# Optimization experiments

Measured on AMD Instinct MI355X. Metric: run time of the kernel, lower is better.

The kernel has to match this reference:

```python
import jax, jax.numpy as jnp
import numpy as np

FM = 80            # feature_maps
N_ROUNDS = 32
NORM_EPS = 1e-3
LOSS_EPS = 1e-8


def _relu6(x):
    return jnp.clip(x, 0.0, 6.0)


def _norm(x):
    # tf.nn.moments over axis 0 + batch_normalization (no scale/offset)
    mean = jnp.mean(x, axis=0, keepdims=True)
    var = jnp.var(x, axis=0, keepdims=True)
    return (x - mean) * jax.lax.rsqrt(var + NORM_EPS)


def setup_inputs() -> dict:
    key = jax.random.key(0)
    n_vars, n_clauses, n_graphs, lits_per_clause = 100000, 420000, 100, 3
    n_cells = n_clauses * lits_per_clause
    ks = jax.random.split(key, 24)

    lit_var = jax.random.randint(ks[0], (n_cells,), 0, n_vars, dtype=jnp.int32)
    lit_neg = jax.random.randint(ks[1], (n_cells,), 0, 2, dtype=jnp.int32)
    clause_idx = jnp.repeat(jnp.arange(n_clauses, dtype=jnp.int32), lits_per_clause)
    clause_graph = jnp.repeat(jnp.arange(n_graphs, dtype=jnp.int32), n_clauses // n_graphs)

    def dense(k, fi, fo):
        return jax.random.normal(k, (fi, fo), jnp.float32) / np.sqrt(fi)

    inp = dict(
        lit_var=lit_var, lit_neg=lit_neg, clause_idx=clause_idx, clause_graph=clause_graph,
        n_vars=n_vars, n_clauses=n_clauses, n_graphs=n_graphs,
        L_init_scale=jnp.float32(1.0 / np.sqrt(FM)),
        C_init_scale=jnp.float32(1.0 / np.sqrt(FM)),
        LC_scale=jnp.float32(0.1), CL_scale=jnp.float32(0.1),
        # L_update MLP: in=3*FM (L, CL_msgs, flip(L)) -> hidden 3*FM relu6 -> FM
        Lu_W0=dense(ks[2], 3 * FM, 3 * FM), Lu_b0=jnp.zeros((3 * FM,), jnp.float32),
        Lu_W1=dense(ks[3], 3 * FM, FM),     Lu_b1=jnp.zeros((FM,), jnp.float32),
        # C_update MLP: in=2*FM (C, LC_msgs) -> hidden 2*FM relu6 -> FM
        Cu_W0=dense(ks[4], 2 * FM, 2 * FM), Cu_b0=jnp.zeros((2 * FM,), jnp.float32),
        Cu_W1=dense(ks[5], 2 * FM, FM),     Cu_b1=jnp.zeros((FM,), jnp.float32),
        # V_score MLP: in=2*FM -> 3 hidden relu6 layers of 2*FM -> 1
        Vs_W0=dense(ks[6], 2 * FM, 2 * FM), Vs_b0=jnp.zeros((2 * FM,), jnp.float32),
        Vs_W1=dense(ks[7], 2 * FM, 2 * FM), Vs_b1=jnp.zeros((2 * FM,), jnp.float32),
        Vs_W2=dense(ks[8], 2 * FM, 2 * FM), Vs_b2=jnp.zeros((2 * FM,), jnp.float32),
        Vs_W3=dense(ks[9], 2 * FM, 1),      Vs_b3=jnp.zeros((1,), jnp.float32),
    )
    return inp


def reference(lit_var, lit_neg, clause_idx, clause_graph, n_vars, n_clauses, n_graphs,
              L_init_scale, C_init_scale, LC_scale, CL_scale,
              Lu_W0, Lu_b0, Lu_W1, Lu_b1,
              Cu_W0, Cu_b0, Cu_W1, Cu_b1,
              Vs_W0, Vs_b0, Vs_W1, Vs_b1, Vs_W2, Vs_b2, Vs_W3, Vs_b3):
    n_lits = 2 * n_vars
    lit_row = lit_var + lit_neg * n_vars          # row in L for each cell
    sign = (1 - 2 * lit_neg).astype(jnp.float32)  # +1 positive literal, -1 negated

    def mlp_L(x):
        return _relu6(x @ Lu_W0 + Lu_b0) @ Lu_W1 + Lu_b1

    def mlp_C(x):
        return _relu6(x @ Cu_W0 + Cu_b0) @ Cu_W1 + Cu_b1

    def v_score(x):
        h = _relu6(x @ Vs_W0 + Vs_b0)
        h = _relu6(h @ Vs_W1 + Vs_b1)
        h = _relu6(h @ Vs_W2 + Vs_b2)
        return h @ Vs_W3 + Vs_b3

    def flip(L):
        return jnp.concatenate([L[n_vars:], L[:n_vars]], axis=0)

    def per_round_loss(logits):
        # softplus_mixed_loss over ragged clauses of signed literals
        lit_vals = logits[lit_var, 0] * sign                         # [n_cells]
        clause_sum = jax.ops.segment_sum(jax.nn.softplus(lit_vals), clause_idx,
                                         num_segments=n_clauses)     # [n_clauses]
        vc = jnp.exp(-clause_sum)
        per_clause = vc * (-jnp.log(1.0 - vc + LOSS_EPS))
        per_graph = jax.ops.segment_sum(per_clause, clause_graph, num_segments=n_graphs)
        return jnp.sum(jnp.sqrt(per_graph + 1e-6))

    L0 = jnp.ones((n_lits, FM), jnp.float32) * L_init_scale
    C0 = jnp.ones((n_clauses, FM), jnp.float32) * C_init_scale

    def round_fn(carry, _):
        L, C, loss = carry
        # CL^T @ L  (sparse gather + segment-sum over clause cells)
        LC_msgs = jax.ops.segment_sum(L[lit_row], clause_idx, num_segments=n_clauses) * LC_scale
        C = _norm(mlp_C(jnp.concatenate([C, LC_msgs], axis=-1)))
        # adj @ C  (scatter-add clause features back to literal rows)
        CL_msgs = jax.ops.segment_sum(C[clause_idx], lit_row, num_segments=n_lits) * CL_scale
        L = _norm(mlp_L(jnp.concatenate([L, CL_msgs, flip(L)], axis=-1)))
        V = jnp.concatenate([L[:n_vars], L[n_vars:]], axis=1)        # [n_vars, 2*FM]
        logits = v_score(V)
        loss = loss + per_round_loss(logits)
        return (L, C, loss), None

    (L, C, loss), _ = jax.lax.scan(round_fn, (L0, C0, jnp.float32(0.0)), None, length=N_ROUNDS)
    # final-round logits (recomputed from the final L state, identical math)
    logits = v_score(jnp.concatenate([L[:n_vars], L[n_vars:]], axis=1))
    return logits, loss / N_ROUNDS
```

## Files before the change

kernel.cpp:

```cpp
#include <hip/hip_runtime.h>
#include <hip/hip_fp8.h>
#include <math.h>


#define NROUNDS 32
#define NORM_EPS 1e-3f
#define LOSS_EPS 1e-8f

static constexpr int NV_CONST = 100000;
static constexpr int NG_CONST = 100;

typedef __attribute__((ext_vector_type(8))) short short8;
typedef __attribute__((ext_vector_type(8))) unsigned char uchar8;
typedef __attribute__((ext_vector_type(16))) unsigned char uchar16;
typedef __attribute__((ext_vector_type(4))) float f32x4;

__device__ __forceinline__ short f2bf(float f) {
    union { float f; unsigned u; } x; x.f = f;
    unsigned r = x.u + 0x7fffu + ((x.u >> 16) & 1u);
    return (short)(r >> 16);
}
__device__ __forceinline__ float bf2f(short s) {
    union { unsigned u; float f; } x; x.u = ((unsigned)(unsigned short)s) << 16;
    return x.f;
}
__device__ __forceinline__ unsigned char f2q8(float f) {
    f = fminf(fmaxf(f, -448.f), 448.f);
    __hip_fp8_e4m3 t(f);
    return t.__x;
}
__device__ __forceinline__ float q82f(unsigned char b) {
    __hip_fp8_e4m3 t; t.__x = b;
    return (float)t;
}


__global__ void k_zero_i(int* __restrict__ p, int n) {
    int i = blockIdx.x * 256 + threadIdx.x;
    if (i < n) p[i] = 0;
}
__global__ void k_fill_b(short* __restrict__ p, int n, const float* __restrict__ vp) {
    int i = blockIdx.x * 256 + threadIdx.x;
    if (i < n) p[i] = f2bf(*vp);
}
__global__ void k_fill_q8(unsigned char* __restrict__ p, int n, const float* __restrict__ vp) {
    int i = blockIdx.x * 256 + threadIdx.x;
    if (i < n) p[i] = f2q8(*vp);
}
__global__ void k_copy_int(int* __restrict__ dst, const int* __restrict__ src, int n) {
    int i = blockIdx.x * 256 + threadIdx.x;
    if (i < n) dst[i] = src[i];
}
__global__ void k_init_slabs(float* __restrict__ slabC, float* __restrict__ slabL,
                             float* __restrict__ loss_a, float nclf) {
    int i = blockIdx.x * 256 + threadIdx.x;
    if (i < 33 * 160) {
        slabC[i] = (i >= 80 && i < 160) ? nclf * (1.f - NORM_EPS) : 0.f;
        slabL[i] = 0.f;
    }
    if (i == 0) loss_a[0] = 0.f;
}

__global__ void k_litrow(const int* __restrict__ lit_var, const int* __restrict__ lit_neg,
                         int* __restrict__ litrow, int* __restrict__ lofs,
                         int* __restrict__ counts, int ncell, int nv) {
    int i = blockIdx.x * 256 + threadIdx.x;
    if (i < ncell) {
        int r = lit_var[i] + lit_neg[i] * nv;
        litrow[i] = r;
        lofs[i] = (r < nv) ? r * 20 : (r - nv) * 20 + 10;
        atomicAdd(&counts[r], 1);
    }
}

__launch_bounds__(1024)
__global__ void k_scan4(const int* __restrict__ counts, int* __restrict__ row_ptr,
                        int n, int total) {
    __shared__ int sd[1024];
    __shared__ int carry;
    int tid = threadIdx.x;
    if (tid == 0) carry = 0;
    __syncthreads();
    for (int base = 0; base < n; base += 4096) {
        int i0 = base + tid * 4;
        int a0 = (i0 + 0 < n) ? counts[i0 + 0] : 0;
        int a1 = (i0 + 1 < n) ? counts[i0 + 1] : 0;
        int a2 = (i0 + 2 < n) ? counts[i0 + 2] : 0;
        int a3 = (i0 + 3 < n) ? counts[i0 + 3] : 0;
        int s = a0 + a1 + a2 + a3;
        sd[tid] = s;
        __syncthreads();
        for (int off = 1; off < 1024; off <<= 1) {
            int t = (tid >= off) ? sd[tid - off] : 0;
            __syncthreads();
            sd[tid] += t;
            __syncthreads();
        }
        int excl = carry + sd[tid] - s;
        if (i0 + 0 < n) row_ptr[i0 + 0] = excl;
        if (i0 + 1 < n) row_ptr[i0 + 1] = excl + a0;
        if (i0 + 2 < n) row_ptr[i0 + 2] = excl + a0 + a1;
        if (i0 + 3 < n) row_ptr[i0 + 3] = excl + a0 + a1 + a2;
        __syncthreads();
        if (tid == 0) carry += sd[1023];
        __syncthreads();
    }
    if (tid == 0) row_ptr[n] = total;
}

__global__ void k_fill_csr(const int* __restrict__ litrow, const int* __restrict__ clause_idx,
                           int* __restrict__ cursor, int* __restrict__ cl_of, int ncell) {
    int i = blockIdx.x * 256 + threadIdx.x;
    if (i < ncell) {
        int r = litrow[i];
        int pos = atomicAdd(&cursor[r], 1);
        cl_of[pos] = clause_idx[i];
    }
}

__global__ void k_pack_w(const float* __restrict__ W, short* __restrict__ Wp,
                         int K, int N, int KB, int NB) {
    int t = blockIdx.x * 256 + threadIdx.x;
    int tot = NB * KB * 64;
    if (t >= tot) return;
    int lane = t & 63;
    int kb = (t >> 6) % KB;
    int nb = t / (64 * KB);
    int quad = lane >> 4, l15 = lane & 15;
    int n = nb * 16 + l15;
#pragma unroll
    for (int j = 0; j < 8; ++j) {
        int k = kb * 32 + quad * 8 + j;
        float f = (k < K && n < N) ? W[(size_t)k * N + n] : 0.f;
        Wp[(size_t)t * 8 + j] = f2bf(f);
    }
}


template <int KB, int NB>
__device__ __forceinline__ void mfma_layer(const short* lds, int SK,
                                           const short8* __restrict__ Wp,
                                           f32x4* acc, int lane, int arow) {
    const int quad8 = (lane >> 4) * 8;
    short8 a[KB];
#pragma unroll
    for (int kb = 0; kb < KB; ++kb)
        a[kb] = *(const short8*)(lds + arow * SK + kb * 32 + quad8);
#pragma unroll
    for (int kb = 0; kb < KB; ++kb)
#pragma unroll
        for (int nb = 0; nb < NB; ++nb)
            acc[nb] = __builtin_amdgcn_mfma_f32_16x16x32_bf16(
                a[kb], Wp[(nb * KB + kb) * 64 + lane], acc[nb], 0, 0, 0);
}

template <int NB>
__device__ __forceinline__ void write_hidden(short* ldsH, int SKH, const f32x4* acc,
                                             const float* __restrict__ bias,
                                             int l15, int quad, int wr0) {
#pragma unroll
    for (int nb = 0; nb < NB; ++nb) {
        int c = nb * 16 + l15;
        float bv = bias[c];
#pragma unroll
        for (int reg = 0; reg < 4; ++reg) {
            int row = wr0 + quad * 4 + reg;
            float v = acc[nb][reg] + bv;
            v = fminf(fmaxf(v, 0.f), 6.f);
            ldsH[row * SKH + c] = f2bf(v);
        }
    }
}

__device__ __forceinline__ void load_stats(const float* __restrict__ slab, float Minv,
                                           float* sS, int tid) {
    if (tid < 80) {
        float m = slab[tid] * Minv;
        float v = slab[80 + tid] * Minv - m * m;
        sS[tid] = m;
        sS[80 + tid] = rsqrtf(v + NORM_EPS);
    }
}

__launch_bounds__(256, 2)
__global__ void k_c_update(short* __restrict__ Cb, unsigned char* __restrict__ Cb8,
                           const unsigned char* __restrict__ Lb8,
                           const int* __restrict__ lofs, const float* __restrict__ scp,
                           const short8* __restrict__ W0p, const float* __restrict__ b0,
                           const short8* __restrict__ W1p, const float* __restrict__ b1,
                           const float* __restrict__ prevSlab, float* __restrict__ nextSlab,
                           float Minv, int ncl) {
    constexpr int SK = 168;
    __shared__ short lds[64 * SK];
    __shared__ float sred[160], sC[160];
    const int lane = threadIdx.x, wy = threadIdx.y, tid = wy * 64 + lane;
    const int r0 = blockIdx.x * 64;
    const int rows = (ncl - r0 < 64) ? (ncl - r0) : 64;

    if (tid < 160) sred[tid] = 0.f;
    load_stats(prevSlab, Minv, sC, tid);
    __syncthreads();

    const float s = *scp;
    const short8* Cbv = (const short8*)Cb;
    const uchar16* Lq = (const uchar16*)Lb8;
    for (int it = tid; it < 64 * 15; it += 256) {
        int lr = it / 15, c = it - lr * 15;
        int cl = r0 + ((lr < rows) ? lr : rows - 1);
        if (c < 10) {
            short8 v = Cbv[(size_t)cl * 10 + c];
            int col = c * 8;
            short8 o;
#pragma unroll
            for (int j = 0; j < 8; ++j)
                o[j] = f2bf((bf2f(v[j]) - sC[col + j]) * sC[80 + col + j]);
            *(short8*)(lds + lr * SK + col) = o;
        } else {
            int cc = c - 10, b = cl * 3;
            int oa = lofs[b] >> 1, ob = lofs[b + 1] >> 1, oc = lofs[b + 2] >> 1;
            uchar16 va = Lq[(size_t)oa + cc];
            uchar16 vb = Lq[(size_t)ob + cc];
            uchar16 vc = Lq[(size_t)oc + cc];
            short8 o0, o1;
#pragma unroll
            for (int j = 0; j < 8; ++j) {
                o0[j] = f2bf((q82f(va[j]) + q82f(vb[j]) + q82f(vc[j])) * s);
                o1[j] = f2bf((q82f(va[8 + j]) + q82f(vb[8 + j]) + q82f(vc[8 + j])) * s);
            }
            *(short8*)(lds + lr * SK + 80 + cc * 16) = o0;
            *(short8*)(lds + lr * SK + 80 + cc * 16 + 8) = o1;
        }
    }
    __syncthreads();

    const int quad = lane >> 4, l15 = lane & 15, wr0 = wy * 16, arow = wr0 + l15;

    f32x4 acc[10];
#pragma unroll
    for (int nb = 0; nb < 10; ++nb) { f32x4 z = {0.f, 0.f, 0.f, 0.f}; acc[nb] = z; }
    mfma_layer<5, 10>(lds, SK, W0p, acc, lane, arow);
    write_hidden<10>(lds, SK, acc, b0, l15, quad, wr0);

    f32x4 acc2[5];
#pragma unroll
    for (int nb = 0; nb < 5; ++nb) { f32x4 z = {0.f, 0.f, 0.f, 0.f}; acc2[nb] = z; }
    mfma_layer<5, 5>(lds, SK, W1p, acc2, lane, arow);

#pragma unroll
    for (int nb = 0; nb < 5; ++nb) {
        int cc = nb * 16 + l15;
        float bv = b1[cc];
        float s1 = 0.f, s2 = 0.f;
#pragma unroll
        for (int reg = 0; reg < 4; ++reg) {
            int lr = wr0 + quad * 4 + reg;
            if (lr < rows) {
                float v = acc2[nb][reg] + bv;
                Cb[(size_t)(r0 + lr) * 80 + cc] = f2bf(v);
                Cb8[(size_t)(r0 + lr) * 80 + cc] = f2q8(v);
                s1 += v; s2 += v * v;
            }
        }
        s1 += __shfl_xor(s1, 16); s1 += __shfl_xor(s1, 32);
        s2 += __shfl_xor(s2, 16); s2 += __shfl_xor(s2, 32);
        if (quad == 0) { atomicAdd(&sred[cc], s1); atomicAdd(&sred[80 + cc], s2); }
    }
    __syncthreads();
    if (tid < 160) atomicAdd(&nextSlab[tid], sred[tid]);
}

__launch_bounds__(256)
__global__ void k_cl_gather(const unsigned char* __restrict__ Cb8,
                            const int* __restrict__ row_ptr,
                            const int* __restrict__ cl_of, const float* __restrict__ scp,
                            const float* __restrict__ slab, float Minv,
                            short* __restrict__ CLb, int nl) {
    __shared__ float sC[160];
    load_stats(slab, Minv, sC, threadIdx.x);
    __syncthreads();
    int idx = blockIdx.x * 256 + threadIdx.x;
    if (idx >= nl * 5) return;
    int r = idx / 5, c16 = idx - r * 5;
    int p0 = row_ptr[r], p1 = row_ptr[r + 1];
    float a[16];
#pragma unroll
    for (int j = 0; j < 16; ++j) a[j] = 0.f;
    const uchar16* Cq = (const uchar16*)Cb8;
    int p = p0;
    for (; p + 4 <= p1; p += 4) {
        int i0 = cl_of[p], i1 = cl_of[p + 1], i2 = cl_of[p + 2], i3 = cl_of[p + 3];
        uchar16 v0 = Cq[(size_t)i0 * 5 + c16];
        uchar16 v1 = Cq[(size_t)i1 * 5 + c16];
        uchar16 v2 = Cq[(size_t)i2 * 5 + c16];
        uchar16 v3 = Cq[(size_t)i3 * 5 + c16];
#pragma unroll
        for (int j = 0; j < 16; ++j)
            a[j] += (q82f(v0[j]) + q82f(v1[j])) + (q82f(v2[j]) + q82f(v3[j]));
    }
    for (; p < p1; ++p) {
        uchar16 v = Cq[(size_t)cl_of[p] * 5 + c16];
#pragma unroll
        for (int j = 0; j < 16; ++j) a[j] += q82f(v[j]);
    }
    float n = (float)(p1 - p0), s = *scp;
    int col = c16 * 16;
    short8 o0, o1;
#pragma unroll
    for (int j = 0; j < 8; ++j) {
        o0[j] = f2bf((a[j] - n * sC[col + j]) * sC[80 + col + j] * s);
        o1[j] = f2bf((a[8 + j] - n * sC[col + 8 + j]) * sC[80 + col + 8 + j] * s);
    }
    ((short8*)CLb)[(size_t)r * 10 + c16 * 2] = o0;
    ((short8*)CLb)[(size_t)r * 10 + c16 * 2 + 1] = o1;
}

__launch_bounds__(256, 2)
__global__ void k_l_update(short* __restrict__ Lraw, const short* __restrict__ Lb,
                           const short* __restrict__ CLb,
                           const short8* __restrict__ W0p, const float* __restrict__ b0,
                           const short8* __restrict__ W1p, const float* __restrict__ b1,
                           float* __restrict__ nextSlab, int nv) {
    constexpr int SK = 264;
    __shared__ short lds[64 * SK];
    __shared__ float sred[160];
    const int lane = threadIdx.x, wy = threadIdx.y, tid = wy * 64 + lane;
    const int vb = blockIdx.x * 32;

    if (tid < 160) sred[tid] = 0.f;
    __syncthreads();

    const short8* Lb8  = (const short8*)Lb;
    const short8* CLb8 = (const short8*)CLb;
    short8 vals[8];
#pragma unroll
    for (int u = 0; u < 8; ++u) {
        int it = tid + u * 256;
        int lr = it >> 5, c = it & 31;
        int v = (lr < 32) ? vb + lr : vb + (lr - 32);
        int half0 = (lr < 32) ? 0 : 10;
        if (c < 10) {
            vals[u] = Lb8[(size_t)v * 20 + half0 + c];
        } else if (c < 20) {
            int r = (lr < 32) ? vb + lr : vb + nv + (lr - 32);
            vals[u] = CLb8[(size_t)r * 10 + (c - 10)];
        } else if (c < 30) {
            vals[u] = Lb8[(size_t)v * 20 + (10 - half0) + (c - 20)];
        } else {
            short8 z = {0, 0, 0, 0, 0, 0, 0, 0};
            vals[u] = z;
        }
    }
#pragma unroll
    for (int u = 0; u < 8; ++u) {
        int it = tid + u * 256;
        int lr = it >> 5, c = it & 31;
        int o = (c < 10) ? c * 8 : (c < 20) ? 80 + (c - 10) * 8
              : (c < 30) ? 160 + (c - 20) * 8 : 240 + (c - 30) * 8;
        *(short8*)(lds + lr * SK + o) = vals[u];
    }
    __syncthreads();

    const int quad = lane >> 4, l15 = lane & 15, wr0 = wy * 16, arow = wr0 + l15;

    f32x4 acc[15];
#pragma unroll
    for (int nb = 0; nb < 15; ++nb) { f32x4 z = {0.f, 0.f, 0.f, 0.f}; acc[nb] = z; }
    mfma_layer<8, 15>(lds, SK, W0p, acc, lane, arow);
    write_hidden<15>(lds, SK, acc, b0, l15, quad, wr0);
    {
        int row = wr0 + (lane >> 2);
        int c = 240 + (lane & 3) * 4;
        short4 z; z.x = 0; z.y = 0; z.z = 0; z.w = 0;
        *(short4*)(lds + row * SK + c) = z;
    }

    f32x4 acc2[5];
#pragma unroll
    for (int nb = 0; nb < 5; ++nb) { f32x4 z = {0.f, 0.f, 0.f, 0.f}; acc2[nb] = z; }
    mfma_layer<8, 5>(lds, SK, W1p, acc2, lane, arow);

#pragma unroll
    for (int nb = 0; nb < 5; ++nb) {
        int cc = nb * 16 + l15;
        float bv = b1[cc];
        float s1 = 0.f, s2 = 0.f;
#pragma unroll
        for (int reg = 0; reg < 4; ++reg) {
            int lr = wr0 + quad * 4 + reg;
            int rabs = (lr < 32) ? vb + lr : vb + nv + (lr - 32);
            float v = acc2[nb][reg] + bv;
            Lraw[(size_t)rabs * 80 + cc] = f2bf(v);
            s1 += v; s2 += v * v;
        }
        s1 += __shfl_xor(s1, 16); s1 += __shfl_xor(s1, 32);
        s2 += __shfl_xor(s2, 16); s2 += __shfl_xor(s2, 32);
        if (quad == 0) { atomicAdd(&sred[cc], s1); atomicAdd(&sred[80 + cc], s2); }
    }
    __syncthreads();
    if (tid < 160) atomicAdd(&nextSlab[tid], sred[tid]);
}

__launch_bounds__(256, 2)
__global__ void k_v_head(const short* __restrict__ Lraw, const float* __restrict__ slab,
                         float Minv,
                         const short8* __restrict__ W0p, const float* __restrict__ b0,
                         const short8* __restrict__ W1p, const float* __restrict__ b1,
                         const short8* __restrict__ W2p, const float* __restrict__ b2,
                         const float* __restrict__ W3, const float* __restrict__ b3,
                         float* __restrict__ logits, short* __restrict__ Lb,
                         unsigned char* __restrict__ Lb8, int nv) {
    constexpr int SK = 168;
    __shared__ short lds[64 * SK];
    __shared__ float sW3[160], sL[160];
    const int lane = threadIdx.x, wy = threadIdx.y, tid = wy * 64 + lane;
    const int v0 = blockIdx.x * 64;
    const int cnt = (nv - v0 < 64) ? (nv - v0) : 64;

    if (tid < 160) sW3[tid] = W3[tid];
    load_stats(slab, Minv, sL, tid);
    __syncthreads();

    const short8* Lraw8 = (const short8*)Lraw;
    short8 vals[5];
#pragma unroll
    for (int u = 0; u < 5; ++u) {
        int it = tid + u * 256;
        int lr = it / 20, c = it - lr * 20;
        int v = v0 + ((lr < cnt) ? lr : cnt - 1);
        int row = (c < 10) ? v : v + nv;
        int cc = (c < 10) ? c : c - 10;
        vals[u] = Lraw8[(size_t)row * 10 + cc];
    }
#pragma unroll
    for (int u = 0; u < 5; ++u) {
        int it = tid + u * 256;
        int lr = it / 20, c = it - lr * 20;
        int v = v0 + ((lr < cnt) ? lr : cnt - 1);
        int cc = (c < 10) ? c : c - 10;
        int col = cc * 8;
        short8 o;
        uchar8 q;
#pragma unroll
        for (int j = 0; j < 8; ++j) {
            float f = (bf2f(vals[u][j]) - sL[col + j]) * sL[80 + col + j];
            o[j] = f2bf(f);
            q[j] = f2q8(f);
        }
        *(short8*)(lds + lr * SK + c * 8) = o;
        if (lr < cnt) {
            *(short8*)(Lb + (size_t)v * 160 + c * 8) = o;
            *(uchar8*)(Lb8 + (size_t)v * 160 + c * 8) = q;
        }
    }
    __syncthreads();

    const int quad = lane >> 4, l15 = lane & 15, wr0 = wy * 16, arow = wr0 + l15;

    f32x4 acc[10];
#pragma unroll
    for (int nb = 0; nb < 10; ++nb) { f32x4 z = {0.f, 0.f, 0.f, 0.f}; acc[nb] = z; }
    mfma_layer<5, 10>(lds, SK, W0p, acc, lane, arow);
    write_hidden<10>(lds, SK, acc, b0, l15, quad, wr0);

#pragma unroll
    for (int nb = 0; nb < 10; ++nb) { f32x4 z = {0.f, 0.f, 0.f, 0.f}; acc[nb] = z; }
    mfma_layer<5, 10>(lds, SK, W1p, acc, lane, arow);
    write_hidden<10>(lds, SK, acc, b1, l15, quad, wr0);

#pragma unroll
    for (int nb = 0; nb < 10; ++nb) { f32x4 z = {0.f, 0.f, 0.f, 0.f}; acc[nb] = z; }
    mfma_layer<5, 10>(lds, SK, W2p, acc, lane, arow);
    write_hidden<10>(lds, SK, acc, b2, l15, quad, wr0);
    __syncthreads();

    int lrow = tid >> 2, t4 = tid & 3;
    float v = 0.f;
    for (int c = t4; c < 160; c += 4) v += bf2f(lds[lrow * SK + c]) * sW3[c];
    v += __shfl_down(v, 2, 4);
    v += __shfl_down(v, 1, 4);
    if (t4 == 0 && lrow < cnt) logits[v0 + lrow] = v + b3[0];
}

__device__ __forceinline__ float softplusf(float x) {
    return fmaxf(x, 0.f) + log1pf(expf(-fabsf(x)));
}

__global__ void k_loss(const float* __restrict__ logits, const int* __restrict__ lit_var,
                       const int* __restrict__ lit_neg, float* __restrict__ loss_acc,
                       int cpg) {
    const int g = blockIdx.x;
    const int tid = threadIdx.x;
    float part = 0.f;
    int cend = (g + 1) * cpg;
    for (int c = g * cpg + tid; c < cend; c += 256) {
        float cs = 0.f;
#pragma unroll
        for (int t = 0; t < 3; ++t) {
            int i = c * 3 + t;
            float sign = lit_neg[i] ? -1.f : 1.f;
            cs += softplusf(logits[lit_var[i]] * sign);
        }
        float vc = expf(-cs);
        part += vc * (-log1pf(LOSS_EPS - vc));
    }
    __shared__ float red[256];
    red[tid] = part;
    __syncthreads();
    for (int s = 128; s > 0; s >>= 1) {
        if (tid < s) red[tid] += red[tid + s];
        __syncthreads();
    }
    if (tid == 0) atomicAdd(loss_acc, sqrtf(red[0] + 1e-6f));
}

__global__ void k_output(float* __restrict__ dout, const float* __restrict__ logits,
                         const float* __restrict__ loss_acc, int nv) {
    int i = blockIdx.x * 256 + threadIdx.x;
    if (i < nv) dout[i] = logits[i];
    else if (i == nv) dout[i] = loss_acc[0] * (1.f / (float)NROUNDS);
}


extern "C" void kernel_launch(void* const* d_in, const int* in_sizes, int n_in,
                              void* d_out, int out_size, void* d_ws, size_t ws_size,
                              hipStream_t stream) {
    const int* lit_var    = (const int*)d_in[0];
    const int* lit_neg    = (const int*)d_in[1];
    const int* clause_idx = (const int*)d_in[2];
    const float* Lscale = (const float*)d_in[7];
    const float* Cscale = (const float*)d_in[8];
    const float* LCs    = (const float*)d_in[9];
    const float* CLs    = (const float*)d_in[10];
    const float* LuW0 = (const float*)d_in[11]; const float* Lub0 = (const float*)d_in[12];
    const float* LuW1 = (const float*)d_in[13]; const float* Lub1 = (const float*)d_in[14];
    const float* CuW0 = (const float*)d_in[15]; const float* Cub0 = (const float*)d_in[16];
    const float* CuW1 = (const float*)d_in[17]; const float* Cub1 = (const float*)d_in[18];
    const float* VsW0 = (const float*)d_in[19]; const float* Vsb0 = (const float*)d_in[20];
    const float* VsW1 = (const float*)d_in[21]; const float* Vsb1 = (const float*)d_in[22];
    const float* VsW2 = (const float*)d_in[23]; const float* Vsb2 = (const float*)d_in[24];
    const float* VsW3 = (const float*)d_in[25]; const float* Vsb3 = (const float*)d_in[26];

    const int ncell = in_sizes[0];
    const int ncl   = in_sizes[3];
    const int nv    = NV_CONST;
    const int nl    = 2 * nv;
    const int ng    = NG_CONST;

    size_t off = 0;
    auto A = [&](size_t bytes) -> void* {
        void* q = (char*)d_ws + off;
        off = (off + bytes + 255) & ~(size_t)255;
        return q;
    };
    short* Cb    = (short*)A((size_t)ncl * 80 * 2);
    short* Lraw  = (short*)A((size_t)nl * 80 * 2);
    short* Lb    = (short*)A((size_t)nv * 160 * 2);
    short* CLb   = (short*)A((size_t)nl * 80 * 2);
    unsigned char* Lb8 = (unsigned char*)A((size_t)nv * 160);
    unsigned char* Cb8 = (unsigned char*)A((size_t)ncl * 80);
    float* logits = (float*)A((size_t)nv * 4);
    float* slabC  = (float*)A(33 * 160 * 4);
    float* slabL  = (float*)A(33 * 160 * 4);
    float* loss_a = (float*)A(256);
    int* litrow  = (int*)A((size_t)ncell * 4);
    int* lofs    = (int*)A((size_t)ncell * 4);
    int* row_ptr = (int*)A((size_t)(nl + 1) * 4);
    int* tmp     = (int*)A((size_t)nl * 4);
    int* cl_of   = (int*)A((size_t)ncell * 4);
    short* CuW0p = (short*)A((size_t)10 * 5 * 64 * 16);
    short* CuW1p = (short*)A((size_t)5  * 5 * 64 * 16);
    short* LuW0p = (short*)A((size_t)15 * 8 * 64 * 16);
    short* LuW1p = (short*)A((size_t)5  * 8 * 64 * 16);
    short* VsW0p = (short*)A((size_t)10 * 5 * 64 * 16);
    short* VsW1p = (short*)A((size_t)10 * 5 * 64 * 16);
    short* VsW2p = (short*)A((size_t)10 * 5 * 64 * 16);

    const dim3 B64x4(64, 4, 1);

    k_zero_i<<<(nl + 255) / 256, 256, 0, stream>>>(tmp, nl);
    k_init_slabs<<<(33 * 160 + 255) / 256, 256, 0, stream>>>(slabC, slabL, loss_a, (float)ncl);
    k_litrow<<<(ncell + 255) / 256, 256, 0, stream>>>(lit_var, lit_neg, litrow, lofs, tmp, ncell, nv);
    k_scan4<<<1, 1024, 0, stream>>>(tmp, row_ptr, nl, ncell);
    k_copy_int<<<(nl + 255) / 256, 256, 0, stream>>>(tmp, row_ptr, nl);
    k_fill_csr<<<(ncell + 255) / 256, 256, 0, stream>>>(litrow, clause_idx, tmp, cl_of, ncell);
    k_fill_b<<<(ncl * 80 + 255) / 256, 256, 0, stream>>>(Cb, ncl * 80, Cscale);
    k_fill_b<<<(nl * 80 + 255) / 256, 256, 0, stream>>>(Lraw, nl * 80, Lscale);
    k_fill_b<<<(nv * 160 + 255) / 256, 256, 0, stream>>>(Lb, nv * 160, Lscale);
    k_fill_q8<<<(nv * 160 + 255) / 256, 256, 0, stream>>>(Lb8, nv * 160, Lscale);
    k_fill_q8<<<(ncl * 80 + 255) / 256, 256, 0, stream>>>(Cb8, ncl * 80, Cscale);
    k_pack_w<<<(10 * 5 * 64 + 255) / 256, 256, 0, stream>>>(CuW0, CuW0p, 160, 160, 5, 10);
    k_pack_w<<<(5  * 5 * 64 + 255) / 256, 256, 0, stream>>>(CuW1, CuW1p, 160, 80, 5, 5);
    k_pack_w<<<(15 * 8 * 64 + 255) / 256, 256, 0, stream>>>(LuW0, LuW0p, 240, 240, 8, 15);
    k_pack_w<<<(5  * 8 * 64 + 255) / 256, 256, 0, stream>>>(LuW1, LuW1p, 240, 80, 8, 5);
    k_pack_w<<<(10 * 5 * 64 + 255) / 256, 256, 0, stream>>>(VsW0, VsW0p, 160, 160, 5, 10);
    k_pack_w<<<(10 * 5 * 64 + 255) / 256, 256, 0, stream>>>(VsW1, VsW1p, 160, 160, 5, 10);
    k_pack_w<<<(10 * 5 * 64 + 255) / 256, 256, 0, stream>>>(VsW2, VsW2p, 160, 160, 5, 10);

    const int cblk  = (ncl + 63) / 64;
    const int lblk  = nv / 32;
    const int vblk  = (nv + 63) / 64;
    const int clblk = (nl * 5 + 255) / 256;
    const float MinvC = 1.f / (float)ncl;
    const float MinvL = 1.f / (float)nl;

    for (int r = 0; r < NROUNDS; ++r) {
        float* sCr  = slabC + (size_t)r * 160;
        float* sCr1 = slabC + (size_t)(r + 1) * 160;
        float* sLr1 = slabL + (size_t)(r + 1) * 160;
        k_c_update<<<cblk, B64x4, 0, stream>>>(
            Cb, Cb8, Lb8, lofs, LCs, (const short8*)CuW0p, Cub0, (const short8*)CuW1p, Cub1,
            sCr, sCr1, MinvC, ncl);
        k_cl_gather<<<clblk, 256, 0, stream>>>(Cb8, row_ptr, cl_of, CLs, sCr1, MinvC, CLb, nl);
        k_l_update<<<lblk, B64x4, 0, stream>>>(
            Lraw, Lb, CLb, (const short8*)LuW0p, Lub0, (const short8*)LuW1p, Lub1, sLr1, nv);
        k_v_head<<<vblk, B64x4, 0, stream>>>(
            Lraw, sLr1, MinvL, (const short8*)VsW0p, Vsb0, (const short8*)VsW1p, Vsb1,
            (const short8*)VsW2p, Vsb2, VsW3, Vsb3, logits, Lb, Lb8, nv);
        k_loss<<<ng, 256, 0, stream>>>(logits, lit_var, lit_neg, loss_a, ncl / ng);
    }

    k_output<<<(nv + 1 + 255) / 256, 256, 0, stream>>>((float*)d_out, logits, loss_a, nv);
}
```

Baseline: 15.57 ms.

## Pad FP8 literal and clause rows to 128 bytes and pack clause offsets

Changes the FP8 copies of L and C so each literal or clause row sits in its own 128-byte line: literals are now indexed per literal row rather than interleaved per variable. The three literal offsets of each clause are stored as a single int4, so k_c_update loads them in one access. The fused C and LC staging loop is split into two branch-free unrolled loops. The aim is aligned, single-line gathers and fewer divergent index computations. The cost is more memory for the padded buffers.

```diff
diff --git a/kernel.cpp b/kernel.cpp
--- a/kernel.cpp
+++ b/kernel.cpp
@@ -62,13 +62,14 @@
 }
 
 __global__ void k_litrow(const int* __restrict__ lit_var, const int* __restrict__ lit_neg,
-                         int* __restrict__ litrow, int* __restrict__ lofs,
+                         int* __restrict__ litrow, int* __restrict__ lofs4,
                          int* __restrict__ counts, int ncell, int nv) {
     int i = blockIdx.x * 256 + threadIdx.x;
     if (i < ncell) {
         int r = lit_var[i] + lit_neg[i] * nv;
         litrow[i] = r;
-        lofs[i] = (r < nv) ? r * 20 : (r - nv) * 20 + 10;
+        int cl = i / 3, t = i - cl * 3;
+        lofs4[cl * 4 + t] = r * 8;
         atomicAdd(&counts[r], 1);
     }
 }
@@ -185,7 +186,7 @@
 __launch_bounds__(256, 2)
 __global__ void k_c_update(short* __restrict__ Cb, unsigned char* __restrict__ Cb8,
                            const unsigned char* __restrict__ Lb8,
-                           const int* __restrict__ lofs, const float* __restrict__ scp,
+                           const int4* __restrict__ lofs4, const float* __restrict__ scp,
                            const short8* __restrict__ W0p, const float* __restrict__ b0,
                            const short8* __restrict__ W1p, const float* __restrict__ b1,
                            const float* __restrict__ prevSlab, float* __restrict__ nextSlab,
@@ -204,29 +205,39 @@
     const float s = *scp;
     const short8* Cbv = (const short8*)Cb;
     const uchar16* Lq = (const uchar16*)Lb8;
-    for (int it = tid; it < 64 * 15; it += 256) {
-        int lr = it / 15, c = it - lr * 15;
+
+#pragma unroll
+    for (int u = 0; u < 3; ++u) {
+        int it = tid + u * 256;
+        int itc = (it < 640) ? it : 639;
+        int lr = itc / 10, c = itc - lr * 10;
         int cl = r0 + ((lr < rows) ? lr : rows - 1);
-        if (c < 10) {
-            short8 v = Cbv[(size_t)cl * 10 + c];
-            int col = c * 8;
-            short8 o;
-#pragma unroll
-            for (int j = 0; j < 8; ++j)
-                o[j] = f2bf((bf2f(v[j]) - sC[col + j]) * sC[80 + col + j]);
+        short8 v = Cbv[(size_t)cl * 10 + c];
+        int col = c * 8;
+        short8 o;
+#pragma unroll
+        for (int j = 0; j < 8; ++j)
+            o[j] = f2bf((bf2f(v[j]) - sC[col + j]) * sC[80 + col + j]);
+        if (it < 640)
             *(short8*)(lds + lr * SK + col) = o;
-        } else {
-            int cc = c - 10, b = cl * 3;
-            int oa = lofs[b] >> 1, ob = lofs[b + 1] >> 1, oc = lofs[b + 2] >> 1;
-            uchar16 va = Lq[(size_t)oa + cc];
-            uchar16 vb = Lq[(size_t)ob + cc];
-            uchar16 vc = Lq[(size_t)oc + cc];
-            short8 o0, o1;
-#pragma unroll
-            for (int j = 0; j < 8; ++j) {
-                o0[j] = f2bf((q82f(va[j]) + q82f(vb[j]) + q82f(vc[j])) * s);
-                o1[j] = f2bf((q82f(va[8 + j]) + q82f(vb[8 + j]) + q82f(vc[8 + j])) * s);
-            }
+    }
+#pragma unroll
+    for (int u = 0; u < 2; ++u) {
+        int it = tid + u * 256;
+        int itc = (it < 320) ? it : 319;
+        int lr = itc / 5, cc = itc - lr * 5;
+        int cl = r0 + ((lr < rows) ? lr : rows - 1);
+        int4 o4 = lofs4[cl];
+        uchar16 va = Lq[(size_t)o4.x + cc];
+        uchar16 vb = Lq[(size_t)o4.y + cc];
+        uchar16 vc = Lq[(size_t)o4.z + cc];
+        short8 o0, o1;
+#pragma unroll
+        for (int j = 0; j < 8; ++j) {
+            o0[j] = f2bf((q82f(va[j]) + q82f(vb[j]) + q82f(vc[j])) * s);
+            o1[j] = f2bf((q82f(va[8 + j]) + q82f(vb[8 + j]) + q82f(vc[8 + j])) * s);
+        }
+        if (it < 320) {
             *(short8*)(lds + lr * SK + 80 + cc * 16) = o0;
             *(short8*)(lds + lr * SK + 80 + cc * 16 + 8) = o1;
         }
@@ -257,7 +268,7 @@
             if (lr < rows) {
                 float v = acc2[nb][reg] + bv;
                 Cb[(size_t)(r0 + lr) * 80 + cc] = f2bf(v);
-                Cb8[(size_t)(r0 + lr) * 80 + cc] = f2q8(v);
+                Cb8[(size_t)(r0 + lr) * 128 + cc] = f2q8(v);
                 s1 += v; s2 += v * v;
             }
         }
@@ -289,16 +300,16 @@
     int p = p0;
     for (; p + 4 <= p1; p += 4) {
         int i0 = cl_of[p], i1 = cl_of[p + 1], i2 = cl_of[p + 2], i3 = cl_of[p + 3];
-        uchar16 v0 = Cq[(size_t)i0 * 5 + c16];
-        uchar16 v1 = Cq[(size_t)i1 * 5 + c16];
-        uchar16 v2 = Cq[(size_t)i2 * 5 + c16];
-        uchar16 v3 = Cq[(size_t)i3 * 5 + c16];
+        uchar16 v0 = Cq[(size_t)i0 * 8 + c16];
+        uchar16 v1 = Cq[(size_t)i1 * 8 + c16];
+        uchar16 v2 = Cq[(size_t)i2 * 8 + c16];
+        uchar16 v3 = Cq[(size_t)i3 * 8 + c16];
 #pragma unroll
         for (int j = 0; j < 16; ++j)
             a[j] += (q82f(v0[j]) + q82f(v1[j])) + (q82f(v2[j]) + q82f(v3[j]));
     }
     for (; p < p1; ++p) {
-        uchar16 v = Cq[(size_t)cl_of[p] * 5 + c16];
+        uchar16 v = Cq[(size_t)cl_of[p] * 8 + c16];
 #pragma unroll
         for (int j = 0; j < 16; ++j) a[j] += q82f(v[j]);
     }
@@ -449,7 +460,8 @@
         *(short8*)(lds + lr * SK + c * 8) = o;
         if (lr < cnt) {
             *(short8*)(Lb + (size_t)v * 160 + c * 8) = o;
-            *(uchar8*)(Lb8 + (size_t)v * 160 + c * 8) = q;
+            int lit = (c < 10) ? v : (v + nv);
+            *(uchar8*)(Lb8 + (size_t)lit * 128 + cc * 8) = q;
         }
     }
     __syncthreads();
@@ -556,14 +568,14 @@
     short* Lraw  = (short*)A((size_t)nl * 80 * 2);
     short* Lb    = (short*)A((size_t)nv * 160 * 2);
     short* CLb   = (short*)A((size_t)nl * 80 * 2);
-    unsigned char* Lb8 = (unsigned char*)A((size_t)nv * 160);
-    unsigned char* Cb8 = (unsigned char*)A((size_t)ncl * 80);
+    unsigned char* Lb8 = (unsigned char*)A((size_t)nl * 128);
+    unsigned char* Cb8 = (unsigned char*)A((size_t)ncl * 128);
     float* logits = (float*)A((size_t)nv * 4);
     float* slabC  = (float*)A(33 * 160 * 4);
     float* slabL  = (float*)A(33 * 160 * 4);
     float* loss_a = (float*)A(256);
     int* litrow  = (int*)A((size_t)ncell * 4);
-    int* lofs    = (int*)A((size_t)ncell * 4);
+    int* lofs4   = (int*)A((size_t)ncl * 16);
     int* row_ptr = (int*)A((size_t)(nl + 1) * 4);
     int* tmp     = (int*)A((size_t)nl * 4);
     int* cl_of   = (int*)A((size_t)ncell * 4);
@@ -579,15 +591,15 @@
 
     k_zero_i<<<(nl + 255) / 256, 256, 0, stream>>>(tmp, nl);
     k_init_slabs<<<(33 * 160 + 255) / 256, 256, 0, stream>>>(slabC, slabL, loss_a, (float)ncl);
-    k_litrow<<<(ncell + 255) / 256, 256, 0, stream>>>(lit_var, lit_neg, litrow, lofs, tmp, ncell, nv);
+    k_litrow<<<(ncell + 255) / 256, 256, 0, stream>>>(lit_var, lit_neg, litrow, lofs4, tmp, ncell, nv);
     k_scan4<<<1, 1024, 0, stream>>>(tmp, row_ptr, nl, ncell);
     k_copy_int<<<(nl + 255) / 256, 256, 0, stream>>>(tmp, row_ptr, nl);
     k_fill_csr<<<(ncell + 255) / 256, 256, 0, stream>>>(litrow, clause_idx, tmp, cl_of, ncell);
     k_fill_b<<<(ncl * 80 + 255) / 256, 256, 0, stream>>>(Cb, ncl * 80, Cscale);
     k_fill_b<<<(nl * 80 + 255) / 256, 256, 0, stream>>>(Lraw, nl * 80, Lscale);
     k_fill_b<<<(nv * 160 + 255) / 256, 256, 0, stream>>>(Lb, nv * 160, Lscale);
-    k_fill_q8<<<(nv * 160 + 255) / 256, 256, 0, stream>>>(Lb8, nv * 160, Lscale);
-    k_fill_q8<<<(ncl * 80 + 255) / 256, 256, 0, stream>>>(Cb8, ncl * 80, Cscale);
+    k_fill_q8<<<(nl * 128 + 255) / 256, 256, 0, stream>>>(Lb8, nl * 128, Lscale);
+    k_fill_q8<<<(ncl * 128 + 255) / 256, 256, 0, stream>>>(Cb8, ncl * 128, Cscale);
     k_pack_w<<<(10 * 5 * 64 + 255) / 256, 256, 0, stream>>>(CuW0, CuW0p, 160, 160, 5, 10);
     k_pack_w<<<(5  * 5 * 64 + 255) / 256, 256, 0, stream>>>(CuW1, CuW1p, 160, 80, 5, 5);
     k_pack_w<<<(15 * 8 * 64 + 255) / 256, 256, 0, stream>>>(LuW0, LuW0p, 240, 240, 8, 15);
@@ -608,8 +620,8 @@
         float* sCr1 = slabC + (size_t)(r + 1) * 160;
         float* sLr1 = slabL + (size_t)(r + 1) * 160;
         k_c_update<<<cblk, B64x4, 0, stream>>>(
-            Cb, Cb8, Lb8, lofs, LCs, (const short8*)CuW0p, Cub0, (const short8*)CuW1p, Cub1,
-            sCr, sCr1, MinvC, ncl);
+            Cb, Cb8, Lb8, (const int4*)lofs4, LCs, (const short8*)CuW0p, Cub0,
+            (const short8*)CuW1p, Cub1, sCr, sCr1, MinvC, ncl);
         k_cl_gather<<<clblk, 256, 0, stream>>>(Cb8, row_ptr, cl_of, CLs, sCr1, MinvC, CLb, nl);
         k_l_update<<<lblk, B64x4, 0, stream>>>(
             Lraw, Lb, CLb, (const short8*)LuW0p, Lub0, (const short8*)LuW1p, Lub1, sLr1, nv);
```

New measurement: 15.69 ms. Within noise of the previous version (+0.7%).
